# Kernel tuning notes

Hardware: AMD Instinct MI355X
Metric: run time of the kernel (lower is better)

The kernel has to match this reference:

```python
import jax, jax.numpy as jnp
import numpy as np

N0, P1 = 10000, 30000
N1 = N0 + P1            # 40000
P2 = 120000
N2 = N1 + P2            # 160000
E0, E1, E2 = 60000, 120000, 480000
IN, H, OUT, K = 3, 192, 3, 2


def setup_inputs() -> dict:
    key = jax.random.key(0)
    k = jax.random.split(key, 13)
    return {
        "features": jax.random.normal(k[0], (N0, IN), jnp.float32),
        "src0": jax.random.randint(k[1], (E0,), 0, N0, jnp.int32),
        "dst0": jax.random.randint(k[2], (E0,), 0, N0, jnp.int32),
        "pool_idx0": jax.random.randint(k[3], (P1, 2), 0, N0, jnp.int32),
        "edge0": jax.random.randint(k[4], (E1, 2), 0, N1, jnp.int32),
        "pool_idx1": jax.random.randint(k[5], (P2, 2), 0, N1, jnp.int32),
        "edge1": jax.random.randint(k[6], (E2, 2), 0, N2, jnp.int32),
        "W_first": 0.3 * jax.random.normal(k[7], (3, (K + 1) * IN, H), jnp.float32),
        "b_first": jnp.zeros((3, H), jnp.float32),
        "W_mid": 0.04 * jax.random.normal(k[8], (3, 12, (K + 1) * H, H), jnp.float32),
        "b_mid": jnp.zeros((3, 12, H), jnp.float32),
        "W_last": 0.05 * jax.random.normal(k[9], (3, (K + 1) * H, OUT), jnp.float32),
        "b_last": jnp.zeros((3, OUT), jnp.float32),
    }


def _norm(dst, n):
    # symmetric-norm factor D^{-1/2}, degrees clamped at 1 (DGL TAGConv)
    deg = jax.ops.segment_sum(jnp.ones(dst.shape[0], jnp.float32), dst, num_segments=n)
    return jnp.clip(deg, 1.0) ** -0.5  # [n]


def _tagconv(x, src, dst, n, norm, W, b):
    fs = [x]
    h = x
    for _ in range(K):
        h = norm[:, None] * jax.ops.segment_sum((h * norm[:, None])[src], dst, num_segments=n)
        fs.append(h)
    return jnp.concatenate(fs, axis=1) @ W + b


def _stage(x, src, dst, n, Wf, bf, Wm, bm, Wl, bl):
    norm = _norm(dst, n)
    h = jax.nn.relu(_tagconv(x, src, dst, n, norm, Wf, bf))
    prev = h  # raw output of previous layer (hidden[-2] in the torch code)
    for i in range(12):
        cur = jax.nn.relu(_tagconv(h, src, dst, n, norm, Wm[i], bm[i]))
        h = 0.5 * (prev + cur) if (i + 1) in (2, 4, 6, 8, 10, 12) else cur
        prev = cur
    return _tagconv(h, src, dst, n, norm, Wl, bl)  # identity activation


def _unpool(feat, pool_idx):
    # new vertex = midpoint of its two parents; appended to the node table
    new_vs = 0.5 * (feat[pool_idx[:, 0]] + feat[pool_idx[:, 1]])
    return jnp.concatenate([feat, new_vs], axis=0)


def _bidir(edge):
    # graph.add_edges(src, dst); graph.add_edges(dst, src)
    return (jnp.concatenate([edge[:, 0], edge[:, 1]]),
            jnp.concatenate([edge[:, 1], edge[:, 0]]))


def reference(features, src0, dst0, pool_idx0, edge0, pool_idx1, edge1,
              W_first, b_first, W_mid, b_mid, W_last, b_last):
    out1 = _stage(features, src0, dst0, N0,
                  W_first[0], b_first[0], W_mid[0], b_mid[0], W_last[0], b_last[0])
    h = _unpool(out1, pool_idx0)            # [N1, 3]
    out1_2 = h
    s1, d1 = _bidir(edge0)
    out2 = _stage(h, s1, d1, N1,
                  W_first[1], b_first[1], W_mid[1], b_mid[1], W_last[1], b_last[1])
    h = _unpool(out2, pool_idx1)            # [N2, 3]
    out2_2 = h
    s2, d2 = _bidir(edge1)
    out3 = _stage(h, s2, d2, N2,
                  W_first[2], b_first[2], W_mid[2], b_mid[2], W_last[2], b_last[2])
    return (out1, out2, out3, out1_2, out2_2)
```

## Files before the change

kernel.cpp:

```cpp
#include <hip/hip_runtime.h>
#include <hip/hip_fp16.h>

#define HF 192

static inline int divup(int a, int b){ return (a+b-1)/b; }

typedef _Float16 half8 __attribute__((ext_vector_type(8)));
typedef float f32x4 __attribute__((ext_vector_type(4)));

#define G_WS_BYTES 195734272ull
__device__ __align__(256) char g_ws[G_WS_BYTES];

#define OFF_HH    0ull
#define OFF_T1H   61440000ull
#define OFF_T2H   122880000ull
#define OFF_DEG  184320000ull
#define OFF_RP   184960000ull
#define OFF_COL  185600032ull
#define OFF_NRM  189440032ull
#define OFF_O1F  190080032ull
#define OFF_U1F  190200032ull
#define OFF_O2F  190680032ull
#define OFF_U2F  191160032ull
#define OFF_WT   193080032ull
#define OFF_X1F  OFF_T1H
#define OFF_X2F  (OFF_T1H + 1920000ull)

__device__ __forceinline__ float*  wsf(unsigned long long o){ return (float*) (g_ws + o); }
__device__ __forceinline__ int*    wsi(unsigned long long o){ return (int*)   (g_ws + o); }
__device__ __forceinline__ __half* wsh(unsigned long long o){ return (__half*)(g_ws + o); }

__global__ void k_zero(unsigned long long off, int n) {
  int i = blockIdx.x*blockDim.x + threadIdx.x;
  if (i < n) wsi(off)[i] = 0;
}
__global__ void k_copyi(unsigned long long aOff, unsigned long long bOff, int n) {
  int i = blockIdx.x*blockDim.x + threadIdx.x;
  if (i < n) wsi(bOff)[i] = wsi(aOff)[i];
}

__global__ void k_count_direct(const int* __restrict__ dst, int E) {
  int* deg = wsi(OFF_DEG);
  int e = blockIdx.x*blockDim.x + threadIdx.x;
  if (e < E) atomicAdd(&deg[dst[e]], 1);
}
__global__ void k_count_bidir(const int* __restrict__ edge, int E) {
  int* deg = wsi(OFF_DEG);
  int e = blockIdx.x*blockDim.x + threadIdx.x;
  if (e < E) {
    atomicAdd(&deg[edge[2*e+1]], 1);
    atomicAdd(&deg[edge[2*e  ]], 1);
  }
}
__global__ void k_norm(int n) {
  const int* deg = wsi(OFF_DEG);
  float* nrm = wsf(OFF_NRM);
  int i = blockIdx.x*blockDim.x + threadIdx.x;
  if (i < n) {
    int d = deg[i]; if (d < 1) d = 1;
    nrm[i] = rsqrtf((float)d);
  }
}
__global__ __launch_bounds__(1024) void k_exscan(int n) {
  const int* in = wsi(OFF_DEG);
  int* out = wsi(OFF_RP);
  __shared__ int sm[1024];
  int t = threadIdx.x;
  int carry = 0;
  for (int base = 0; base < n; base += 4096) {
    int idx = base + t*4;
    int v0 = (idx+0 < n) ? in[idx+0] : 0;
    int v1 = (idx+1 < n) ? in[idx+1] : 0;
    int v2 = (idx+2 < n) ? in[idx+2] : 0;
    int v3 = (idx+3 < n) ? in[idx+3] : 0;
    int s = v0+v1+v2+v3;
    sm[t] = s;
    __syncthreads();
    for (int off = 1; off < 1024; off <<= 1) {
      int u = (t >= off) ? sm[t-off] : 0;
      __syncthreads();
      sm[t] += u;
      __syncthreads();
    }
    int excl = carry + sm[t] - s;
    if (idx   < n) out[idx]   = excl;
    if (idx+1 < n) out[idx+1] = excl + v0;
    if (idx+2 < n) out[idx+2] = excl + v0+v1;
    if (idx+3 < n) out[idx+3] = excl + v0+v1+v2;
    carry += sm[1023];
    __syncthreads();
  }
  if (t == 0) out[n] = carry;
}
__global__ void k_fill_direct(const int* __restrict__ src, const int* __restrict__ dst, int E) {
  int* cur = wsi(OFF_DEG);
  int* col = wsi(OFF_COL);
  int e = blockIdx.x*blockDim.x + threadIdx.x;
  if (e < E) {
    int p = atomicAdd(&cur[dst[e]], 1);
    col[p] = src[e];
  }
}
__global__ void k_fill_bidir(const int* __restrict__ edge, int E) {
  int* cur = wsi(OFF_DEG);
  int* col = wsi(OFF_COL);
  int e = blockIdx.x*blockDim.x + threadIdx.x;
  if (e < E) {
    int u = edge[2*e], v = edge[2*e+1];
    int p = atomicAdd(&cur[v], 1); col[p] = u;
    int q = atomicAdd(&cur[u], 1); col[q] = v;
  }
}

__global__ void k_spmm3(const float* __restrict__ Xext, unsigned long long Xoff,
                        unsigned long long Yoff, int n) {
  const float* X = Xext ? Xext : wsf(Xoff);
  float* Y = wsf(Yoff);
  const int* rowptr = wsi(OFF_RP);
  const int* col = wsi(OFF_COL);
  const float* nrm = wsf(OFF_NRM);
  int row = blockIdx.x*blockDim.x + threadIdx.x;
  if (row >= n) return;
  int s = rowptr[row], e = rowptr[row+1];
  float a0=0.f, a1=0.f, a2=0.f;
  for (int i = s; i < e; ++i) {
    int c = col[i]; float v = nrm[c];
    a0 = fmaf(v, X[c*3+0], a0);
    a1 = fmaf(v, X[c*3+1], a1);
    a2 = fmaf(v, X[c*3+2], a2);
  }
  float nm = nrm[row];
  Y[row*3+0] = a0*nm; Y[row*3+1] = a1*nm; Y[row*3+2] = a2*nm;
}

__global__ __launch_bounds__(192) void k_spmm8(unsigned long long Xoff,
                                               unsigned long long Yoff, int n) {
  int gid = blockIdx.x*192 + threadIdx.x;
  if (gid >= n*24) return;
  int row = gid / 24, f8 = gid - row*24;
  const half8* __restrict__ X8 = (const half8*)wsh(Xoff);
  half8* __restrict__ Y8 = (half8*)wsh(Yoff);
  const int* rowptr = wsi(OFF_RP);
  const int* col = wsi(OFF_COL);
  const float* nrm = wsf(OFF_NRM);
  int s = rowptr[row], e = rowptr[row+1];
  float acc0[8], acc1[8];
  #pragma unroll
  for (int j = 0; j < 8; ++j) { acc0[j] = 0.f; acc1[j] = 0.f; }
  int i = s;
  for (; i + 2 <= e; i += 2) {
    int c0 = col[i], c1 = col[i+1];
    float w0 = nrm[c0], w1 = nrm[c1];
    half8 v0 = X8[(size_t)c0*24 + f8];
    half8 v1 = X8[(size_t)c1*24 + f8];
    #pragma unroll
    for (int j = 0; j < 8; ++j) {
      acc0[j] = fmaf(w0, (float)v0[j], acc0[j]);
      acc1[j] = fmaf(w1, (float)v1[j], acc1[j]);
    }
  }
  if (i < e) {
    int c0 = col[i];
    float w0 = nrm[c0];
    half8 v0 = X8[(size_t)c0*24 + f8];
    #pragma unroll
    for (int j = 0; j < 8; ++j) acc0[j] = fmaf(w0, (float)v0[j], acc0[j]);
  }
  float nm = nrm[row];
  half8 r;
  #pragma unroll
  for (int j = 0; j < 8; ++j) r[j] = (_Float16)((acc0[j] + acc1[j])*nm);
  Y8[(size_t)row*24 + f8] = r;
}

__global__ void k_gemm_first(const float* __restrict__ xext, unsigned long long xOff,
                             const float* __restrict__ W, const float* __restrict__ b, int n) {
  const float* x  = xext ? xext : wsf(xOff);
  const float* x1 = wsf(OFF_X1F);
  const float* x2 = wsf(OFF_X2F);
  __half* H = wsh(OFF_HH);
  int idx = blockIdx.x*blockDim.x + threadIdx.x;
  if (idx >= n*HF) return;
  int row = idx / HF, c = idx - row*HF;
  float acc = b[c];
  #pragma unroll
  for (int k = 0; k < 3; ++k) acc = fmaf(x [row*3+k], W[(0+k)*HF + c], acc);
  #pragma unroll
  for (int k = 0; k < 3; ++k) acc = fmaf(x1[row*3+k], W[(3+k)*HF + c], acc);
  #pragma unroll
  for (int k = 0; k < 3; ++k) acc = fmaf(x2[row*3+k], W[(6+k)*HF + c], acc);
  H[idx] = __float2half(fmaxf(acc, 0.f));
}

__global__ void k_wprep(const float* __restrict__ Wm, int s) {
  int idx = blockIdx.x*blockDim.x + threadIdx.x;
  if (idx >= 12*576*HF) return;
  int it = idx / (576*HF);
  int rem = idx - it*576*HF;
  int k = rem / HF;
  int c = rem - k*HF;
  wsh(OFF_WT)[(size_t)it*HF*576 + (size_t)c*576 + k] =
      __float2half(Wm[((size_t)(s*12+it)*576 + k)*HF + c]);
}

#define BPAD 104
__global__ __launch_bounds__(256,4) void k_mfma_mid(
    const float* __restrict__ b, int it, int n, int residual)
{
  __half* __restrict__ H = wsh(OFF_HH);
  const __half* __restrict__ T1 = wsh(OFF_T1H);
  const __half* __restrict__ T2 = wsh(OFF_T2H);
  const __half* __restrict__ Wt = wsh(OFF_WT) + (size_t)it*HF*576;
  __shared__ _Float16 Bs[192*BPAD];
  int t = threadIdx.x;
  int w = t >> 6;
  int l = t & 63;
  int lr = l & 15;
  int lg = l >> 4;
  int row0 = blockIdx.x*128 + w*32;

  f32x4 acc[2][12];
  #pragma unroll
  for (int s2 = 0; s2 < 2; ++s2)
    #pragma unroll
    for (int i = 0; i < 12; ++i) acc[s2][i] = (f32x4){0.f,0.f,0.f,0.f};

  const __half* Xp[3] = { H, T1, T2 };
  for (int p = 0; p < 3; ++p) {
    const __half* X = Xp[p];
    for (int kh = 0; kh < 2; ++kh) {
      __syncthreads();
      for (int i = t; i < 192*12; i += 256) {
        int c  = i / 12;
        int k8 = i - c*12;
        *(half8*)&Bs[c*BPAD + k8*8] =
            *(const half8*)&Wt[(size_t)c*576 + p*HF + kh*96 + k8*8];
      }
      __syncthreads();
      #pragma unroll
      for (int k0 = 0; k0 < 96; k0 += 32) {
        half8 a0 = *(const half8*)&X[(size_t)(row0 + lr     )*HF + kh*96 + k0 + lg*8];
        half8 a1 = *(const half8*)&X[(size_t)(row0 + 16 + lr)*HF + kh*96 + k0 + lg*8];
        #pragma unroll
        for (int tl = 0; tl < 12; ++tl) {
          half8 bb = *(const half8*)&Bs[(tl*16 + lr)*BPAD + k0 + lg*8];
          acc[0][tl] = __builtin_amdgcn_mfma_f32_16x16x32_f16(a0, bb, acc[0][tl], 0, 0, 0);
          acc[1][tl] = __builtin_amdgcn_mfma_f32_16x16x32_f16(a1, bb, acc[1][tl], 0, 0, 0);
        }
      }
    }
  }

  #pragma unroll
  for (int s2 = 0; s2 < 2; ++s2) {
    #pragma unroll
    for (int tl = 0; tl < 12; ++tl) {
      int c = tl*16 + lr;
      float bias = b[c];
      #pragma unroll
      for (int j = 0; j < 4; ++j) {
        int row = row0 + s2*16 + lg*4 + j;
        if (row < n) {
          size_t o = (size_t)row*HF + c;
          float cur = fmaxf(acc[s2][tl][j] + bias, 0.f);
          float h = cur;
          if (residual) h = 0.5f*(__half2float(H[o]) + cur);
          H[o] = __float2half(h);
        }
      }
    }
  }
}

__global__ void k_last_lin(const float* __restrict__ W, const float* __restrict__ b,
                           float* __restrict__ outb, unsigned long long outfOff,
                           int hasOutf, int n) {
  int row = blockIdx.x*blockDim.x + threadIdx.x;
  if (row >= n) return;
  const __half* bufs[3] = { wsh(OFF_HH), wsh(OFF_T1H), wsh(OFF_T2H) };
  float a0 = b[0], a1 = b[1], a2 = b[2];
  for (int p = 0; p < 3; ++p) {
    const half8* x8 = (const half8*)&bufs[p][(size_t)row*HF];
    #pragma unroll 4
    for (int k8 = 0; k8 < 24; ++k8) {
      half8 v = x8[k8];
      #pragma unroll
      for (int j = 0; j < 8; ++j) {
        int k = k8*8 + j;
        const float* w = &W[(p*HF + k)*3];
        float vv = (float)v[j];
        a0 = fmaf(vv, w[0], a0); a1 = fmaf(vv, w[1], a1); a2 = fmaf(vv, w[2], a2);
      }
    }
  }
  outb[row*3+0] = a0;
  outb[row*3+1] = a1;
  outb[row*3+2] = a2;
  if (hasOutf) {
    float* outf = wsf(outfOff);
    outf[row*3+0] = a0; outf[row*3+1] = a1; outf[row*3+2] = a2;
  }
}

__global__ void k_unpool(unsigned long long srcOff, const int* __restrict__ pidx,
                         unsigned long long dstfOff, float* __restrict__ dstb,
                         int n, int P) {
  const float* src = wsf(srcOff);
  float* dstf = wsf(dstfOff);
  int i = blockIdx.x*blockDim.x + threadIdx.x;
  if (i >= n + P) return;
  float v0, v1, v2;
  if (i < n) {
    v0 = src[i*3+0]; v1 = src[i*3+1]; v2 = src[i*3+2];
  } else {
    int a = pidx[(i-n)*2], c = pidx[(i-n)*2+1];
    v0 = 0.5f*(src[a*3+0] + src[c*3+0]);
    v1 = 0.5f*(src[a*3+1] + src[c*3+1]);
    v2 = 0.5f*(src[a*3+2] + src[c*3+2]);
  }
  dstf[i*3+0] = v0; dstf[i*3+1] = v1; dstf[i*3+2] = v2;
  dstb[i*3+0] = v0;
  dstb[i*3+1] = v1;
  dstb[i*3+2] = v2;
}

extern "C" void kernel_launch(void* const* d_in, const int* in_sizes, int n_in,
                              void* d_out, int out_size, void* d_ws, size_t ws_size,
                              hipStream_t stream) {
  (void)in_sizes; (void)n_in; (void)out_size; (void)d_ws; (void)ws_size;
  const float* features = (const float*)d_in[0];
  const int*  src0  = (const int*)d_in[1];
  const int*  dst0  = (const int*)d_in[2];
  const int*  pool0 = (const int*)d_in[3];
  const int*  edge0 = (const int*)d_in[4];
  const int*  pool1 = (const int*)d_in[5];
  const int*  edge1 = (const int*)d_in[6];
  const float* Wf = (const float*)d_in[7];
  const float* bfp = (const float*)d_in[8];
  const float* Wm = (const float*)d_in[9];
  const float* bm = (const float*)d_in[10];
  const float* Wl = (const float*)d_in[11];
  const float* bl = (const float*)d_in[12];
  float* out = (float*)d_out;

  auto csr = [&](int n, const int* srcD, const int* dstD, int Edir,
                 const int* edgeB, int Eund) {
    k_zero<<<divup(n,256),256,0,stream>>>(OFF_DEG, n);
    if (srcD) k_count_direct<<<divup(Edir,256),256,0,stream>>>(dstD, Edir);
    else      k_count_bidir <<<divup(Eund,256),256,0,stream>>>(edgeB, Eund);
    k_norm<<<divup(n,256),256,0,stream>>>(n);
    k_exscan<<<1,1024,0,stream>>>(n);
    k_copyi<<<divup(n,256),256,0,stream>>>(OFF_RP, OFF_DEG, n);
    if (srcD) k_fill_direct<<<divup(Edir,256),256,0,stream>>>(srcD, dstD, Edir);
    else      k_fill_bidir <<<divup(Eund,256),256,0,stream>>>(edgeB, Eund);
  };

  auto stage_u = [&](const float* xext, unsigned long long xOff, int n,
                     const int* srcD, const int* dstD, int Edir,
                     const int* edgeB, int Eund,
                     int s, float* outb, unsigned long long outfOff, int hasOutf) {
    csr(n, srcD, dstD, Edir, edgeB, Eund);
    k_wprep<<<divup(12*576*HF,256),256,0,stream>>>(Wm, s);
    k_spmm3<<<divup(n,256),256,0,stream>>>(xext, xOff, OFF_X1F, n);
    k_spmm3<<<divup(n,256),256,0,stream>>>(nullptr, OFF_X1F, OFF_X2F, n);
    k_gemm_first<<<divup(n*HF,256),256,0,stream>>>(xext, xOff,
        Wf + (size_t)s*9*HF, bfp + s*HF, n);
    int gsp = divup(n*24,192);
    for (int it = 0; it < 12; ++it) {
      k_spmm8<<<gsp,192,0,stream>>>(OFF_HH,  OFF_T1H, n);
      k_spmm8<<<gsp,192,0,stream>>>(OFF_T1H, OFF_T2H, n);
      k_mfma_mid<<<divup(n,128),256,0,stream>>>(bm + (s*12+it)*HF, it, n,
          ((it+1)%2==0) ? 1 : 0);
    }
    k_spmm8<<<gsp,192,0,stream>>>(OFF_HH,  OFF_T1H, n);
    k_spmm8<<<gsp,192,0,stream>>>(OFF_T1H, OFF_T2H, n);
    k_last_lin<<<divup(n,256),256,0,stream>>>(Wl + (size_t)s*576*3, bl + s*3,
        outb, outfOff, hasOutf, n);
  };

  stage_u(features, 0ull, 10000, src0, dst0, 60000, nullptr, 0,
          0, out + 0, OFF_O1F, 1);
  k_unpool<<<divup(40000,256),256,0,stream>>>(OFF_O1F, pool0, OFF_U1F, out + 630000, 10000, 30000);
  stage_u(nullptr, OFF_U1F, 40000, nullptr, nullptr, 0, edge0, 120000,
          1, out + 30000, OFF_O2F, 1);
  k_unpool<<<divup(160000,256),256,0,stream>>>(OFF_O2F, pool1, OFF_U2F, out + 750000, 40000, 120000);
  stage_u(nullptr, OFF_U2F, 160000, nullptr, nullptr, 0, edge1, 480000,
          2, out + 150000, OFF_O1F, 0);
}
```

Before: 6.055 ms.

## Halve MFMA row tile per wave and unroll SpMM gather loop by four

The mid-layer MFMA GEMM now gives each wave 16 rows instead of 32, so a block covers 64 rows and the grid doubles. Accumulator registers drop, and the launch-bounds occupancy hint is removed. In exchange, the shared-memory weight tile is loaded twice as often per row and each B fragment is reused half as much. Separately, the SpMM gather loop now processes four neighbors per iteration to get more independent loads in flight.

```diff
diff --git a/kernel.cpp b/kernel.cpp
--- a/kernel.cpp
+++ b/kernel.cpp
@@ -148,6 +148,21 @@
   #pragma unroll
   for (int j = 0; j < 8; ++j) { acc0[j] = 0.f; acc1[j] = 0.f; }
   int i = s;
+  for (; i + 4 <= e; i += 4) {
+    int c0 = col[i], c1 = col[i+1], c2 = col[i+2], c3 = col[i+3];
+    float w0 = nrm[c0], w1 = nrm[c1], w2 = nrm[c2], w3 = nrm[c3];
+    half8 v0 = X8[(size_t)c0*24 + f8];
+    half8 v1 = X8[(size_t)c1*24 + f8];
+    half8 v2 = X8[(size_t)c2*24 + f8];
+    half8 v3 = X8[(size_t)c3*24 + f8];
+    #pragma unroll
+    for (int j = 0; j < 8; ++j) {
+      acc0[j] = fmaf(w0, (float)v0[j], acc0[j]);
+      acc1[j] = fmaf(w1, (float)v1[j], acc1[j]);
+      acc0[j] = fmaf(w2, (float)v2[j], acc0[j]);
+      acc1[j] = fmaf(w3, (float)v3[j], acc1[j]);
+    }
+  }
   for (; i + 2 <= e; i += 2) {
     int c0 = col[i], c1 = col[i+1];
     float w0 = nrm[c0], w1 = nrm[c1];
@@ -204,7 +219,7 @@
 }
 
 #define BPAD 104
-__global__ __launch_bounds__(256,4) void k_mfma_mid(
+__global__ __launch_bounds__(256) void k_mfma_mid(
     const float* __restrict__ b, int it, int n, int residual)
 {
   __half* __restrict__ H = wsh(OFF_HH);
@@ -217,13 +232,11 @@
   int l = t & 63;
   int lr = l & 15;
   int lg = l >> 4;
-  int row0 = blockIdx.x*128 + w*32;
-
-  f32x4 acc[2][12];
-  #pragma unroll
-  for (int s2 = 0; s2 < 2; ++s2)
-    #pragma unroll
-    for (int i = 0; i < 12; ++i) acc[s2][i] = (f32x4){0.f,0.f,0.f,0.f};
+  int row0 = blockIdx.x*64 + w*16;
+
+  f32x4 acc[12];
+  #pragma unroll
+  for (int i = 0; i < 12; ++i) acc[i] = (f32x4){0.f,0.f,0.f,0.f};
 
   const __half* Xp[3] = { H, T1, T2 };
   for (int p = 0; p < 3; ++p) {
@@ -239,34 +252,29 @@
       __syncthreads();
       #pragma unroll
       for (int k0 = 0; k0 < 96; k0 += 32) {
-        half8 a0 = *(const half8*)&X[(size_t)(row0 + lr     )*HF + kh*96 + k0 + lg*8];
-        half8 a1 = *(const half8*)&X[(size_t)(row0 + 16 + lr)*HF + kh*96 + k0 + lg*8];
+        half8 a = *(const half8*)&X[(size_t)(row0 + lr)*HF + kh*96 + k0 + lg*8];
         #pragma unroll
         for (int tl = 0; tl < 12; ++tl) {
           half8 bb = *(const half8*)&Bs[(tl*16 + lr)*BPAD + k0 + lg*8];
-          acc[0][tl] = __builtin_amdgcn_mfma_f32_16x16x32_f16(a0, bb, acc[0][tl], 0, 0, 0);
-          acc[1][tl] = __builtin_amdgcn_mfma_f32_16x16x32_f16(a1, bb, acc[1][tl], 0, 0, 0);
+          acc[tl] = __builtin_amdgcn_mfma_f32_16x16x32_f16(a, bb, acc[tl], 0, 0, 0);
         }
       }
     }
   }
 
   #pragma unroll
-  for (int s2 = 0; s2 < 2; ++s2) {
+  for (int tl = 0; tl < 12; ++tl) {
+    int c = tl*16 + lr;
+    float bias = b[c];
     #pragma unroll
-    for (int tl = 0; tl < 12; ++tl) {
-      int c = tl*16 + lr;
-      float bias = b[c];
-      #pragma unroll
-      for (int j = 0; j < 4; ++j) {
-        int row = row0 + s2*16 + lg*4 + j;
-        if (row < n) {
-          size_t o = (size_t)row*HF + c;
-          float cur = fmaxf(acc[s2][tl][j] + bias, 0.f);
-          float h = cur;
-          if (residual) h = 0.5f*(__half2float(H[o]) + cur);
-          H[o] = __float2half(h);
-        }
+    for (int j = 0; j < 4; ++j) {
+      int row = row0 + lg*4 + j;
+      if (row < n) {
+        size_t o = (size_t)row*HF + c;
+        float cur = fmaxf(acc[tl][j] + bias, 0.f);
+        float h = cur;
+        if (residual) h = 0.5f*(__half2float(H[o]) + cur);
+        H[o] = __float2half(h);
       }
     }
   }
@@ -369,7 +377,7 @@
     for (int it = 0; it < 12; ++it) {
       k_spmm8<<<gsp,192,0,stream>>>(OFF_HH,  OFF_T1H, n);
       k_spmm8<<<gsp,192,0,stream>>>(OFF_T1H, OFF_T2H, n);
-      k_mfma_mid<<<divup(n,128),256,0,stream>>>(bm + (s*12+it)*HF, it, n,
+      k_mfma_mid<<<divup(n,64),256,0,stream>>>(bm + (s*12+it)*HF, it, n,
           ((it+1)%2==0) ? 1 : 0);
     }
     k_spmm8<<<gsp,192,0,stream>>>(OFF_HH,  OFF_T1H, n);
```

Measured after the change: 5.519 ms. -8.9%, faster.
